# Kernel tuning notes

Hardware: AMD Instinct MI355X
Metric: run time of the kernel (lower is better)

Reference implementation:

```python
import jax, jax.numpy as jnp
import numpy as np

HIDDEN = 64
N_HEADS = 4
TOP_K = 10
ALPHA = 0.3


def setup_inputs() -> dict:
    key = jax.random.key(0)
    ks = jax.random.split(key, 12)
    B, N, T, Dd, Ds, H = 4, 2048, 32, 16, 8, HIDDEN
    s = lambda i, shape, scale: (jax.random.normal(ks[i], shape, dtype=jnp.float32) * scale)
    return {
        "x_dyn": jax.random.normal(ks[0], (B, N, T, Dd), dtype=jnp.float32),
        "x_stat": jax.random.normal(ks[1], (B, N, Ds), dtype=jnp.float32),
        "A_prior": jax.random.uniform(ks[2], (B, N, N), dtype=jnp.float32),
        "W_dyn": s(3, (Dd, H), 1.0 / np.sqrt(Dd)),
        "b_dyn": jnp.zeros((H,), jnp.float32),
        "W_stat": s(4, (Ds, H), 1.0 / np.sqrt(Ds)),
        "b_stat": jnp.zeros((H,), jnp.float32),
        "W_fuse": s(5, (2 * H, H), 1.0 / np.sqrt(2 * H)),
        "b_fuse": jnp.zeros((H,), jnp.float32),
        "Wq": s(6, (H, H), 1.0 / np.sqrt(H)),
        "Wk": s(7, (H, H), 1.0 / np.sqrt(H)),
    }


def reference(x_dyn, x_stat, A_prior, W_dyn, b_dyn, W_stat, b_stat, W_fuse, b_fuse, Wq, Wk):
    B, N = x_dyn.shape[0], x_dyn.shape[1]
    H, nh = HIDDEN, N_HEADS
    dh = H // nh

    # TemporalEncoder: linear + mean over time + ReLU -> (B, N, H)
    h = jax.nn.relu(jnp.mean(x_dyn @ W_dyn + b_dyn, axis=2))
    # FeatureEncoder: linear + ReLU -> (B, N, H)
    h_s = jax.nn.relu(x_stat @ W_stat + b_stat)
    # Fusion
    h = jnp.concatenate([h, h_s], axis=-1) @ W_fuse + b_fuse

    # GraphAttention: multi-head softmax(QK^T / sqrt(dh)) averaged over heads
    q = (h @ Wq).reshape(B, N, nh, dh)
    k = (h @ Wk).reshape(B, N, nh, dh)
    scores = jnp.einsum("bnhd,bmhd->bhnm", q, k) / jnp.sqrt(jnp.float32(dh))
    A_learn = jnp.mean(jax.nn.softmax(scores, axis=-1), axis=1)  # (B, N, N)

    # Top-k mask along last dim (scatter 1s at topk indices)
    _, topk_inds = jax.lax.top_k(A_learn, TOP_K)  # (B, N, k)
    b_idx = jnp.arange(B)[:, None, None]
    n_idx = jnp.arange(N)[None, :, None]
    mask = jnp.zeros_like(A_learn).at[b_idx, n_idx, topk_inds].set(1.0)
    A_sparse = A_learn * mask
    A_learn = (A_sparse + jnp.swapaxes(A_sparse, 1, 2)) * 0.5

    # Blend with prior
    A_final = ALPHA * A_prior + (1.0 - ALPHA) * A_learn

    # Laplacian L = D - A
    degree = jnp.sum(A_final, axis=-1)  # (B, N)
    eye = jnp.eye(N, dtype=A_final.dtype)
    L = degree[..., None] * eye - A_final
    return (L, A_final)
```

## Files before the change

### kernel.cpp

```cpp
#include <hip/hip_runtime.h>

#define NBATCH 4
#define NN 2048
#define NR 8192
#define TOPK 10
#define COLSW 2054

typedef __attribute__((ext_vector_type(16))) float f32x16;
typedef __attribute__((ext_vector_type(8))) short bf16x8;

__device__ inline unsigned short f2bf(float x) {
    unsigned u = __float_as_uint(x);
    unsigned r = (u + 0x7FFF + ((u >> 16) & 1)) >> 16;
    return (unsigned short)r;
}

__global__ __launch_bounds__(256) void k1_encode(
    const float* __restrict__ xd, const float* __restrict__ xs,
    const float* __restrict__ Wd, const float* __restrict__ bd,
    const float* __restrict__ Ws, const float* __restrict__ bs,
    const float* __restrict__ Wf, const float* __restrict__ bf,
    const float* __restrict__ Wq, const float* __restrict__ Wk,
    unsigned short* __restrict__ qh, unsigned short* __restrict__ kh)
{
    int wave = threadIdx.x >> 6;
    int lane = threadIdx.x & 63;
    int r = blockIdx.x * 4 + wave;

    __shared__ float xm[4][16];
    __shared__ float xst[4][8];
    __shared__ float hc[4][128];
    __shared__ float hh[4][64];

    const float* xdr = xd + (size_t)r * 512;
    float acc = 0.f;
    #pragma unroll
    for (int j = 0; j < 8; ++j) acc += xdr[lane + 64*j];
    acc += __shfl_xor(acc, 16);
    acc += __shfl_xor(acc, 32);
    if (lane < 16) xm[wave][lane] = acc * (1.0f/32.0f);
    if (lane < 8)  xst[wave][lane] = xs[(size_t)r*8 + lane];
    __syncthreads();

    float a1 = bd[lane];
    #pragma unroll
    for (int d = 0; d < 16; ++d) a1 += xm[wave][d] * Wd[d*64 + lane];
    a1 = fmaxf(a1, 0.f);
    float a2 = bs[lane];
    #pragma unroll
    for (int d = 0; d < 8; ++d) a2 += xst[wave][d] * Ws[d*64 + lane];
    a2 = fmaxf(a2, 0.f);
    hc[wave][lane] = a1;
    hc[wave][64 + lane] = a2;
    __syncthreads();

    float hv0 = bf[lane], hv1 = 0.f, hv2 = 0.f, hv3 = 0.f;
    #pragma unroll
    for (int j = 0; j < 128; j += 4) {
        hv0 += hc[wave][j]   * Wf[(j)*64   + lane];
        hv1 += hc[wave][j+1] * Wf[(j+1)*64 + lane];
        hv2 += hc[wave][j+2] * Wf[(j+2)*64 + lane];
        hv3 += hc[wave][j+3] * Wf[(j+3)*64 + lane];
    }
    hh[wave][lane] = (hv0 + hv1) + (hv2 + hv3);
    __syncthreads();

    float qv0 = 0.f, qv1 = 0.f, kv0 = 0.f, kv1 = 0.f;
    #pragma unroll
    for (int j = 0; j < 64; j += 2) {
        float h0 = hh[wave][j], h1 = hh[wave][j+1];
        qv0 += h0 * Wq[(j)*64   + lane];
        qv1 += h1 * Wq[(j+1)*64 + lane];
        kv0 += h0 * Wk[(j)*64   + lane];
        kv1 += h1 * Wk[(j+1)*64 + lane];
    }
    float qv = qv0 + qv1, kv = kv0 + kv1;
    int b = r >> 11, n = r & 2047;
    int head = lane >> 4, dim = lane & 15;
    size_t base = ((size_t)(b*4 + head) * NN + n) * 16;
    qh[base + dim] = f2bf(qv);
    kh[base + dim] = f2bf(kv);
}

__global__ __launch_bounds__(256) void k3_base(
    const float* __restrict__ prior, float* __restrict__ Lout,
    float* __restrict__ Aout)
{
    int r = blockIdx.x;
    const float4* pr = (const float4*)(prior + (size_t)r * NN);
    float4* Ar = (float4*)(Aout + (size_t)r * NN);
    float4* Lr = (float4*)(Lout + (size_t)r * NN);
    float sum = 0.f;
    for (int i = threadIdx.x; i < NN/4; i += 256) {
        float4 p = pr[i];
        float4 a; a.x = 0.3f*p.x; a.y = 0.3f*p.y; a.z = 0.3f*p.z; a.w = 0.3f*p.w;
        Ar[i] = a;
        float4 lv; lv.x = -a.x; lv.y = -a.y; lv.z = -a.z; lv.w = -a.w;
        Lr[i] = lv;
        sum += a.x + a.y + a.z + a.w;
    }
    #pragma unroll
    for (int o = 32; o > 0; o >>= 1) sum += __shfl_down(sum, o);
    __shared__ float wsum[4];
    if ((threadIdx.x & 63) == 0) wsum[threadIdx.x >> 6] = sum;
    __syncthreads();
    if (threadIdx.x == 0) {
        float tot = wsum[0] + wsum[1] + wsum[2] + wsum[3];
        atomicAdd(&Lout[(size_t)r * NN + (r & 2047)], tot);
    }
}

__global__ __launch_bounds__(1024, 4) void k2_fused(
    const unsigned short* __restrict__ qh, const unsigned short* __restrict__ kh,
    float* __restrict__ Lout, float* __restrict__ Aout)
{
    const float C1 = 0.36067376022224085f;
    int b  = blockIdx.x >> 6;
    int rg = blockIdx.x & 63;
    int tid = threadIdx.x;
    int w = tid >> 6, l = tid & 63;
    int row = l & 31, khalf = l >> 5;

    __shared__ unsigned short vt[32][COLSW];
    __shared__ float redS[16][4][32];
    __shared__ float r4s[4][32];

    bf16x8 qfrag[4];
    #pragma unroll
    for (int h = 0; h < 4; ++h)
        qfrag[h] = *(const bf16x8*)(qh + ((size_t)(b*4+h) * NN + rg*32 + row) * 16 + khalf*8);

    float Sl[4] = {0.f, 0.f, 0.f, 0.f};
    for (int t = 0; t < 4; ++t) {
        int m0 = w*128 + t*32;
        #pragma unroll
        for (int h = 0; h < 4; ++h) {
            bf16x8 kfrag = *(const bf16x8*)(kh + ((size_t)(b*4+h) * NN + m0 + row) * 16 + khalf*8);
            f32x16 acc = {0.f,0.f,0.f,0.f,0.f,0.f,0.f,0.f,0.f,0.f,0.f,0.f,0.f,0.f,0.f,0.f};
            acc = __builtin_amdgcn_mfma_f32_32x32x16_bf16(kfrag, qfrag[h], acc, 0, 0, 0);
            #pragma unroll
            for (int rr = 0; rr < 16; ++rr) Sl[h] += exp2f(acc[rr] * C1);
        }
    }
    #pragma unroll
    for (int h = 0; h < 4; ++h) Sl[h] += __shfl_xor(Sl[h], 32);
    if (l < 32) {
        #pragma unroll
        for (int h = 0; h < 4; ++h) redS[w][h][l] = Sl[h];
    }
    __syncthreads();
    if (tid < 128) {
        int h = tid >> 5, rw = tid & 31;
        float s = 0.f;
        #pragma unroll
        for (int ww = 0; ww < 16; ++ww) s += redS[ww][h][rw];
        r4s[h][rw] = 0.25f / s;
    }
    __syncthreads();

    float r4[4];
    #pragma unroll
    for (int h = 0; h < 4; ++h) r4[h] = r4s[h][row];

    for (int t = 0; t < 4; ++t) {
        int m0 = w*128 + t*32;
        float vacc[16];
        #pragma unroll
        for (int rr = 0; rr < 16; ++rr) vacc[rr] = 0.f;
        #pragma unroll
        for (int h = 0; h < 4; ++h) {
            bf16x8 kfrag = *(const bf16x8*)(kh + ((size_t)(b*4+h) * NN + m0 + row) * 16 + khalf*8);
            f32x16 acc = {0.f,0.f,0.f,0.f,0.f,0.f,0.f,0.f,0.f,0.f,0.f,0.f,0.f,0.f,0.f,0.f};
            acc = __builtin_amdgcn_mfma_f32_32x32x16_bf16(kfrag, qfrag[h], acc, 0, 0, 0);
            #pragma unroll
            for (int rr = 0; rr < 16; ++rr)
                vacc[rr] = fmaf(exp2f(acc[rr] * C1), r4[h], vacc[rr]);
        }
        #pragma unroll
        for (int p = 0; p < 8; ++p) {
            int reg0 = p*2;
            int c = m0 + ((reg0 & 3) + 8*(reg0 >> 2) + 4*khalf);
            unsigned pk = (unsigned)f2bf(vacc[reg0]) | ((unsigned)f2bf(vacc[reg0+1]) << 16);
            *(unsigned*)&vt[row][c] = pk;
        }
    }
    __syncthreads();

    #pragma unroll 1
    for (int rr2 = 0; rr2 < 2; ++rr2) {
        int prow = w*2 + rr2;
        unsigned tk[TOPK];
        #pragma unroll
        for (int s = 0; s < TOPK; ++s) tk[s] = 0u;
        for (int j = 0; j < 16; ++j) {
            int m1 = 2*l + 128*j;
            unsigned pair = *(const unsigned*)&vt[prow][m1];
            unsigned key0 = (pair << 16)          | (unsigned)(2047 - m1);
            unsigned key1 = (pair & 0xFFFF0000u)  | (unsigned)(2046 - m1);
            if (key0 > tk[TOPK-1]) {
                unsigned ck = key0;
                #pragma unroll
                for (int s = 0; s < TOPK; ++s) {
                    bool ins = ck > tk[s];
                    unsigned o = tk[s];
                    tk[s] = ins ? ck : o;
                    ck    = ins ? o  : ck;
                }
            }
            if (key1 > tk[TOPK-1]) {
                unsigned ck = key1;
                #pragma unroll
                for (int s = 0; s < TOPK; ++s) {
                    bool ins = ck > tk[s];
                    unsigned o = tk[s];
                    tk[s] = ins ? ck : o;
                    ck    = ins ? o  : ck;
                }
            }
        }
        unsigned mykey = 0u;
        #pragma unroll 1
        for (int s = 0; s < TOPK; ++s) {
            unsigned kmax = tk[0];
            #pragma unroll
            for (int d = 1; d < 64; d <<= 1) {
                unsigned o = __shfl_xor(kmax, d);
                kmax = (o > kmax) ? o : kmax;
            }
            if (tk[0] == kmax) {
                #pragma unroll
                for (int q = 0; q < TOPK-1; ++q) tk[q] = tk[q+1];
                tk[TOPK-1] = 0u;
            }
            if (l == s) mykey = kmax;
        }

        int n = rg*32 + prow;
        size_t rbase = (size_t)(b*NN + n) * NN;
        float wv = 0.f;
        int j = 0;
        if (l < TOPK) {
            wv = 0.35f * __uint_as_float(mykey & 0xFFFF0000u);
            j = 2047 - (int)(mykey & 0x7FFu);
        }
        float swv = wv;
        #pragma unroll
        for (int d = 1; d <= 8; d <<= 1) swv += __shfl_xor(swv, d);
        if (l == 0) atomicAdd(&Lout[rbase + n], swv);
        if (l < TOPK) {
            size_t jbase = (size_t)(b*NN + j) * NN;
            atomicAdd(&Aout[rbase + j],  wv);
            atomicAdd(&Aout[jbase + n],  wv);
            atomicAdd(&Lout[rbase + j], -wv);
            atomicAdd(&Lout[jbase + n], -wv);
            atomicAdd(&Lout[jbase + j],  wv);
        }
    }
}

extern "C" void kernel_launch(void* const* d_in, const int* in_sizes, int n_in,
                              void* d_out, int out_size, void* d_ws, size_t ws_size,
                              hipStream_t stream)
{
    const float* xd    = (const float*)d_in[0];
    const float* xs    = (const float*)d_in[1];
    const float* prior = (const float*)d_in[2];
    const float* Wd    = (const float*)d_in[3];
    const float* bd    = (const float*)d_in[4];
    const float* Ws    = (const float*)d_in[5];
    const float* bs    = (const float*)d_in[6];
    const float* Wf    = (const float*)d_in[7];
    const float* bf    = (const float*)d_in[8];
    const float* Wq    = (const float*)d_in[9];
    const float* Wk    = (const float*)d_in[10];

    float* Lout = (float*)d_out;
    float* Aout = Lout + (size_t)NR * NN;

    unsigned short* qh = (unsigned short*)d_ws;
    unsigned short* kh = qh + (size_t)16 * NN * 16;

    k1_encode<<<NR/4, 256, 0, stream>>>(xd, xs, Wd, bd, Ws, bs, Wf, bf, Wq, Wk, qh, kh);
    k3_base<<<NR, 256, 0, stream>>>(prior, Lout, Aout);
    k2_fused<<<NBATCH*64, 1024, 0, stream>>>(qh, kh, Lout, Aout);
}
```

Baseline: 322.3 us.

## Fuse encoder with prior-blend kernel and keep per-thread top-k candidates in registers

The encoder and prior-blend/Laplacian-base kernels are merged into one launch, with extra blocks handling the prior rows. This removes one kernel launch and lets the two independent workloads overlap. In the attention kernel, each thread now keeps a running top-10 of its own softmax-averaged values in registers. It writes only those candidates to shared memory, instead of storing the full bf16 row and scanning it afterwards. This shrinks shared memory use and the final per-row scan, at the cost of divergent register insertion work inside the main loop.

New measurement: 324.0 us. Within noise of the previous version (+0.5%).

```diff
diff --git a/kernel.cpp b/kernel.cpp
--- a/kernel.cpp
+++ b/kernel.cpp
@@ -4,7 +4,7 @@
 #define NN 2048
 #define NR 8192
 #define TOPK 10
-#define COLSW 2054
+#define CSTRIDE 321
 
 typedef __attribute__((ext_vector_type(16))) float f32x16;
 typedef __attribute__((ext_vector_type(8))) short bf16x8;
@@ -15,14 +15,42 @@
     return (unsigned short)r;
 }
 
-__global__ __launch_bounds__(256) void k1_encode(
+__global__ __launch_bounds__(256) void k13(
     const float* __restrict__ xd, const float* __restrict__ xs,
     const float* __restrict__ Wd, const float* __restrict__ bd,
     const float* __restrict__ Ws, const float* __restrict__ bs,
     const float* __restrict__ Wf, const float* __restrict__ bf,
     const float* __restrict__ Wq, const float* __restrict__ Wk,
-    unsigned short* __restrict__ qh, unsigned short* __restrict__ kh)
+    unsigned short* __restrict__ qh, unsigned short* __restrict__ kh,
+    const float* __restrict__ prior, float* __restrict__ Lout,
+    float* __restrict__ Aout)
 {
+    if (blockIdx.x >= NR/4) {
+        int r = blockIdx.x - NR/4;
+        __shared__ float wsum[4];
+        const float4* pr = (const float4*)(prior + (size_t)r * NN);
+        float4* Ar = (float4*)(Aout + (size_t)r * NN);
+        float4* Lr = (float4*)(Lout + (size_t)r * NN);
+        float sum = 0.f;
+        for (int i = threadIdx.x; i < NN/4; i += 256) {
+            float4 p = pr[i];
+            float4 a; a.x = 0.3f*p.x; a.y = 0.3f*p.y; a.z = 0.3f*p.z; a.w = 0.3f*p.w;
+            Ar[i] = a;
+            float4 lv; lv.x = -a.x; lv.y = -a.y; lv.z = -a.z; lv.w = -a.w;
+            Lr[i] = lv;
+            sum += a.x + a.y + a.z + a.w;
+        }
+        #pragma unroll
+        for (int o = 32; o > 0; o >>= 1) sum += __shfl_down(sum, o);
+        if ((threadIdx.x & 63) == 0) wsum[threadIdx.x >> 6] = sum;
+        __syncthreads();
+        if (threadIdx.x == 0) {
+            float tot = wsum[0] + wsum[1] + wsum[2] + wsum[3];
+            atomicAdd(&Lout[(size_t)r * NN + (r & 2047)], tot);
+        }
+        return;
+    }
+
     int wave = threadIdx.x >> 6;
     int lane = threadIdx.x & 63;
     int r = blockIdx.x * 4 + wave;
@@ -80,34 +108,6 @@
     size_t base = ((size_t)(b*4 + head) * NN + n) * 16;
     qh[base + dim] = f2bf(qv);
     kh[base + dim] = f2bf(kv);
-}
-
-__global__ __launch_bounds__(256) void k3_base(
-    const float* __restrict__ prior, float* __restrict__ Lout,
-    float* __restrict__ Aout)
-{
-    int r = blockIdx.x;
-    const float4* pr = (const float4*)(prior + (size_t)r * NN);
-    float4* Ar = (float4*)(Aout + (size_t)r * NN);
-    float4* Lr = (float4*)(Lout + (size_t)r * NN);
-    float sum = 0.f;
-    for (int i = threadIdx.x; i < NN/4; i += 256) {
-        float4 p = pr[i];
-        float4 a; a.x = 0.3f*p.x; a.y = 0.3f*p.y; a.z = 0.3f*p.z; a.w = 0.3f*p.w;
-        Ar[i] = a;
-        float4 lv; lv.x = -a.x; lv.y = -a.y; lv.z = -a.z; lv.w = -a.w;
-        Lr[i] = lv;
-        sum += a.x + a.y + a.z + a.w;
-    }
-    #pragma unroll
-    for (int o = 32; o > 0; o >>= 1) sum += __shfl_down(sum, o);
-    __shared__ float wsum[4];
-    if ((threadIdx.x & 63) == 0) wsum[threadIdx.x >> 6] = sum;
-    __syncthreads();
-    if (threadIdx.x == 0) {
-        float tot = wsum[0] + wsum[1] + wsum[2] + wsum[3];
-        atomicAdd(&Lout[(size_t)r * NN + (r & 2047)], tot);
-    }
 }
 
 __global__ __launch_bounds__(1024, 4) void k2_fused(
@@ -121,7 +121,7 @@
     int w = tid >> 6, l = tid & 63;
     int row = l & 31, khalf = l >> 5;
 
-    __shared__ unsigned short vt[32][COLSW];
+    __shared__ unsigned cand[32 * CSTRIDE];
     __shared__ float redS[16][4][32];
     __shared__ float r4s[4][32];
 
@@ -162,6 +162,9 @@
     #pragma unroll
     for (int h = 0; h < 4; ++h) r4[h] = r4s[h][row];
 
+    unsigned tkl[TOPK];
+    #pragma unroll
+    for (int s = 0; s < TOPK; ++s) tkl[s] = 0u;
     for (int t = 0; t < 4; ++t) {
         int m0 = w*128 + t*32;
         float vacc[16];
@@ -177,60 +180,48 @@
                 vacc[rr] = fmaf(exp2f(acc[rr] * C1), r4[h], vacc[rr]);
         }
         #pragma unroll
-        for (int p = 0; p < 8; ++p) {
-            int reg0 = p*2;
-            int c = m0 + ((reg0 & 3) + 8*(reg0 >> 2) + 4*khalf);
-            unsigned pk = (unsigned)f2bf(vacc[reg0]) | ((unsigned)f2bf(vacc[reg0+1]) << 16);
-            *(unsigned*)&vt[row][c] = pk;
-        }
+        for (int rr = 0; rr < 16; ++rr) {
+            int c = m0 + ((rr & 3) + 8*(rr >> 2) + 4*khalf);
+            unsigned key = ((unsigned)f2bf(vacc[rr]) << 16) | (unsigned)(2047 - c);
+            if (key > tkl[TOPK-1]) {
+                unsigned ck = key;
+                #pragma unroll
+                for (int s = 0; s < TOPK; ++s) {
+                    bool ins = ck > tkl[s];
+                    unsigned o = tkl[s];
+                    tkl[s] = ins ? ck : o;
+                    ck     = ins ? o  : ck;
+                }
+            }
+        }
+    }
+    {
+        unsigned* cr = &cand[row * CSTRIDE + (w*2 + khalf) * TOPK];
+        #pragma unroll
+        for (int s = 0; s < TOPK; ++s) cr[s] = tkl[s];
     }
     __syncthreads();
 
     #pragma unroll 1
     for (int rr2 = 0; rr2 < 2; ++rr2) {
         int prow = w*2 + rr2;
-        unsigned tk[TOPK];
-        #pragma unroll
-        for (int s = 0; s < TOPK; ++s) tk[s] = 0u;
-        for (int j = 0; j < 16; ++j) {
-            int m1 = 2*l + 128*j;
-            unsigned pair = *(const unsigned*)&vt[prow][m1];
-            unsigned key0 = (pair << 16)          | (unsigned)(2047 - m1);
-            unsigned key1 = (pair & 0xFFFF0000u)  | (unsigned)(2046 - m1);
-            if (key0 > tk[TOPK-1]) {
-                unsigned ck = key0;
-                #pragma unroll
-                for (int s = 0; s < TOPK; ++s) {
-                    bool ins = ck > tk[s];
-                    unsigned o = tk[s];
-                    tk[s] = ins ? ck : o;
-                    ck    = ins ? o  : ck;
-                }
-            }
-            if (key1 > tk[TOPK-1]) {
-                unsigned ck = key1;
-                #pragma unroll
-                for (int s = 0; s < TOPK; ++s) {
-                    bool ins = ck > tk[s];
-                    unsigned o = tk[s];
-                    tk[s] = ins ? ck : o;
-                    ck    = ins ? o  : ck;
-                }
-            }
-        }
+        const unsigned* flat = &cand[prow * CSTRIDE];
+        unsigned tk5[5];
+        #pragma unroll
+        for (int i = 0; i < 5; ++i) tk5[i] = flat[l*5 + i];
         unsigned mykey = 0u;
         #pragma unroll 1
         for (int s = 0; s < TOPK; ++s) {
-            unsigned kmax = tk[0];
+            unsigned kmax = tk5[0];
             #pragma unroll
             for (int d = 1; d < 64; d <<= 1) {
                 unsigned o = __shfl_xor(kmax, d);
                 kmax = (o > kmax) ? o : kmax;
             }
-            if (tk[0] == kmax) {
+            if (tk5[0] == kmax) {
                 #pragma unroll
-                for (int q = 0; q < TOPK-1; ++q) tk[q] = tk[q+1];
-                tk[TOPK-1] = 0u;
+                for (int q = 0; q < 4; ++q) tk5[q] = tk5[q+1];
+                tk5[4] = 0u;
             }
             if (l == s) mykey = kmax;
         }
@@ -280,7 +271,7 @@
     unsigned short* qh = (unsigned short*)d_ws;
     unsigned short* kh = qh + (size_t)16 * NN * 16;
 
-    k1_encode<<<NR/4, 256, 0, stream>>>(xd, xs, Wd, bd, Ws, bs, Wf, bf, Wq, Wk, qh, kh);
-    k3_base<<<NR, 256, 0, stream>>>(prior, Lout, Aout);
+    k13<<<NR/4 + NR, 256, 0, stream>>>(xd, xs, Wd, bd, Ws, bs, Wf, bf, Wq, Wk,
+                                       qh, kh, prior, Lout, Aout);
     k2_fused<<<NBATCH*64, 1024, 0, stream>>>(qh, kh, Lout, Aout);
 }
```
